# Optimization experiments

Hardware: AMD Instinct MI355X
Metric: run time of the kernel (lower is better)

The kernel has to match this reference:

```python
import math
import jax, jax.numpy as jnp
import numpy as np

S, B, H = 2048, 1, 4096
NH, HD = 32, 128          # heads, head dim
ROT = HD // 2             # rotary dim per 2D-RoPE half = 64


def rotate_half(x):
    x1, x2 = jnp.split(x, 2, axis=-1)
    return jnp.concatenate([-x2, x1], axis=-1)


def rope_tables(seq_len, dim, base=10000.0):
    inv_freq = 1.0 / (base ** (jnp.arange(0, dim, 2, dtype=jnp.float32) / dim))
    freqs = jnp.arange(seq_len, dtype=jnp.float32)[:, None] * inv_freq[None, :]
    emb = jnp.concatenate([freqs, freqs], axis=-1)  # [S, dim]
    return jnp.cos(emb), jnp.sin(emb)


def apply_rope(q, k, cos, sin, pos):
    # q,k: [S,B,NH,ROT]; pos: [S,B] -> gather cos/sin per token
    c = cos[pos][:, :, None, :]  # [S,B,1,ROT]
    s = sin[pos][:, :, None, :]
    return q * c + rotate_half(q) * s, k * c + rotate_half(k) * s


def setup_inputs() -> dict:
    key = jax.random.key(0)
    ks = jax.random.split(key, 5)
    hidden_states = jax.random.normal(ks[0], (S, B, H), dtype=jnp.float32)
    pos = jnp.arange(S, dtype=jnp.int64 if jax.config.jax_enable_x64 else jnp.int32)
    position_ids = jnp.stack([pos, pos])[None]  # [B=1, 2, S]
    attention_mask = jnp.triu(jnp.ones((S, S), dtype=bool), k=1)[None, None]  # True = masked
    scale = 0.02
    wqkv = jax.random.normal(ks[1], (3 * H, H), dtype=jnp.float32) * scale
    bqkv = jax.random.normal(ks[2], (3 * H,), dtype=jnp.float32) * scale
    wdense = jax.random.normal(ks[3], (H, H), dtype=jnp.float32) * scale
    bdense = jax.random.normal(ks[4], (H,), dtype=jnp.float32) * scale
    return {"hidden_states": hidden_states, "position_ids": position_ids,
            "attention_mask": attention_mask, "wqkv": wqkv, "bqkv": bqkv,
            "wdense": wdense, "bdense": bdense, "layer_id": 1}


def reference(hidden_states, position_ids, attention_mask, wqkv, bqkv, wdense, bdense, layer_id):
    s, b, h = hidden_states.shape
    # fused QKV projection: [S,B,NH,3*HD]
    mixed = (jnp.einsum('sbh,oh->sbo', hidden_states, wqkv) + bqkv).reshape(s, b, NH, 3 * HD)
    q, k, v = jnp.split(mixed, 3, axis=-1)  # each [S,B,NH,HD]

    # 2D RoPE: split head dim in half, rotate each half with its own position ids
    q1, q2 = jnp.split(q, 2, axis=-1)
    k1, k2 = jnp.split(k, 2, axis=-1)
    cos, sin = rope_tables(s, ROT)
    pos = position_ids[:, 0, :].T       # [S,B]
    block_pos = position_ids[:, 1, :].T  # [S,B]
    q1, k1 = apply_rope(q1, k1, cos, sin, pos)
    q2, k2 = apply_rope(q2, k2, cos, sin, block_pos)
    q = jnp.concatenate([q1, q2], axis=-1)
    k = jnp.concatenate([k1, k2], axis=-1)

    # layer-scaled attention (ChatGLM style)
    coeff = float(layer_id + 1)
    q = q / (math.sqrt(HD) * coeff)
    scores = jnp.einsum('sbhd,tbhd->bhst', q, k)  # [B,NH,S,S]
    scores = jnp.where(attention_mask, jnp.float32(-10000.0), scores)
    scores = scores.astype(jnp.float32) * coeff
    probs = jax.nn.softmax(scores, axis=-1).astype(q.dtype)
    context = jnp.einsum('bhst,tbhd->sbhd', probs, v).reshape(s, b, h)

    out = jnp.einsum('sbh,oh->sbo', context, wdense) + bdense
    return out
```

## Files before the change

### kernel.cpp

```cpp
#include <hip/hip_runtime.h>

typedef unsigned short u16;
typedef unsigned int u32;
typedef __attribute__((ext_vector_type(4))) float f32x4;
typedef __attribute__((ext_vector_type(8))) short bf16x8;
typedef __attribute__((ext_vector_type(2))) unsigned int u32x2;

#define S_LEN 2048
#define NHEAD 32
#define HDD 128
#define HID 4096
#define N_QKV 12288
#define KDIM 4096
#define RS 12288

__device__ __forceinline__ u16 f2bf(float f) {
  u32 u = __builtin_bit_cast(u32, f);
  u = (u + 0x7FFFu + ((u >> 16) & 1u)) >> 16;
  return (u16)u;
}
__device__ __forceinline__ float bf2f(u16 h) {
  u32 u = ((u32)h) << 16;
  return __builtin_bit_cast(float, u);
}

__device__ __forceinline__ void gl2lds16(const void* g, void* l) {
  __builtin_amdgcn_global_load_lds(
      (const __attribute__((address_space(1))) u32*)g,
      (__attribute__((address_space(3))) u32*)l, 16, 0, 0);
}

#define FULL_BAR()                          \
  {                                         \
    asm volatile("" ::: "memory");          \
    __builtin_amdgcn_s_barrier();           \
    asm volatile("" ::: "memory");          \
  }

__global__ __launch_bounds__(256) void cvt3_kernel(const float* __restrict__ s0, u16* __restrict__ d0, int n0,
                                                   const float* __restrict__ s1, u16* __restrict__ d1, int n1,
                                                   const float* __restrict__ s2, u16* __restrict__ d2, int n2,
                                                   float* __restrict__ cos_t, float* __restrict__ sin_t) {
  int i = blockIdx.x * blockDim.x + threadIdx.x;
  if (i < S_LEN * 32) {
    int s = i >> 5, ii = i & 31;
    float invf = expf(-0.28782313662425572f * (float)ii);
    float a = (float)s * invf;
    cos_t[i] = cosf(a);
    sin_t[i] = sinf(a);
  }
  int st = gridDim.x * blockDim.x;
  int ntot = n0 + n1 + n2;
  for (; i < ntot; i += st) {
    const float* s;
    u16* d;
    int j = i;
    if (j < n0) {
      s = s0; d = d0;
    } else if (j < n0 + n1) {
      j -= n0; s = s1; d = d1;
    } else {
      j -= n0 + n1; s = s2; d = d2;
    }
    float4 v = ((const float4*)s)[j];
    u32x2 o;
    o.x = (u32)f2bf(v.x) | ((u32)f2bf(v.y) << 16);
    o.y = (u32)f2bf(v.z) | ((u32)f2bf(v.w) << 16);
    ((u32x2*)d)[j] = o;
  }
}

__global__ __launch_bounds__(512, 2) void gemmQ(const u16* __restrict__ A,
                                                const u16* __restrict__ B,
                                                const float* __restrict__ bias,
                                                u16* __restrict__ outb) {
  __shared__ __align__(16) char lds[3][40960];

  const int tid = threadIdx.x;
  const int lane = tid & 63, w = tid >> 6;
  const int l15 = lane & 15, g = lane >> 4;
  const int wm = w >> 2, wn = w & 3;

  int x = blockIdx.x & 7, loc = blockIdx.x >> 3;
  int mb = loc & 7, nb = x * 4 + (loc >> 3);
  const int bm = mb * 256, bn = nb * 384;

  f32x4 acc[8][6];
  f32x4 z4 = {0.f, 0.f, 0.f, 0.f};
#pragma unroll
  for (int mi = 0; mi < 8; ++mi)
#pragma unroll
    for (int ni = 0; ni < 6; ++ni) acc[mi][ni] = z4;

  const size_t K2 = (size_t)KDIM * 2;

  const char* gA[2];
#pragma unroll
  for (int j = 0; j < 2; ++j) {
    int slot = j * 512 + tid;
    int line = slot >> 3;
    int sl = (slot & 7) ^ (line & 7);
    int row = 2 * line + (sl >> 2);
    int colb = (sl & 3) * 16;
    gA[j] = (const char*)A + (size_t)(bm + row) * K2 + colb;
  }
  const char* gB[3];
#pragma unroll
  for (int j = 0; j < 3; ++j) {
    int slot = j * 512 + tid;
    int line = slot >> 3;
    int sl = (slot & 7) ^ (line & 7);
    int row = 2 * line + (sl >> 2);
    int colb = (sl & 3) * 16;
    gB[j] = (const char*)B + (size_t)(bn + row) * K2 + colb;
  }
  const int ldst = w * 1024;

#define QIA(t, bi)                                                  \
  {                                                                 \
    char* Lb = lds[bi];                                             \
    gl2lds16(gA[0] + (size_t)(t) * 64, Lb + ldst);                  \
    gl2lds16(gA[1] + (size_t)(t) * 64, Lb + 8192 + ldst);           \
  }
#define QIB(t, bi)                                                  \
  {                                                                 \
    char* Lb = lds[bi] + 16384;                                     \
    _Pragma("unroll")                                               \
    for (int j = 0; j < 3; ++j)                                     \
      gl2lds16(gB[j] + (size_t)(t) * 64, Lb + j * 8192 + ldst);     \
  }

  int offA[8], offB[6];
#pragma unroll
  for (int mi = 0; mi < 8; ++mi) {
    int r = wm * 128 + mi * 16 + l15;
    int line = r >> 1;
    int sl = (((r & 1) << 2) + g) ^ (line & 7);
    offA[mi] = line * 128 + sl * 16;
  }
#pragma unroll
  for (int ni = 0; ni < 6; ++ni) {
    int r = wn * 96 + ni * 16 + l15;
    int line = r >> 1;
    int sl = (((r & 1) << 2) + g) ^ (line & 7);
    offB[ni] = 16384 + line * 128 + sl * 16;
  }

  QIA(0, 0); QIB(0, 0);
  QIA(1, 1); QIB(1, 1);
  asm volatile("s_waitcnt vmcnt(5)" ::: "memory");
  FULL_BAR();

  int cur = 0, nx2 = 2;
  for (int kt = 0; kt < 128; ++kt) {
    const char* buf = lds[cur];
    const bool pf = (kt + 2) < 128;
    bf16x8 a[4], b[6];
#pragma unroll
    for (int mi = 0; mi < 4; ++mi) a[mi] = *(const bf16x8*)(buf + offA[mi]);
#pragma unroll
    for (int ni = 0; ni < 6; ++ni) b[ni] = *(const bf16x8*)(buf + offB[ni]);
    if (pf) QIA(kt + 2, nx2);
    FULL_BAR();
    __builtin_amdgcn_s_setprio(1);
#pragma unroll
    for (int mi = 0; mi < 4; ++mi)
#pragma unroll
      for (int ni = 0; ni < 6; ++ni)
        acc[mi][ni] = __builtin_amdgcn_mfma_f32_16x16x32_bf16(a[mi], b[ni], acc[mi][ni], 0, 0, 0);
    __builtin_amdgcn_s_setprio(0);
#pragma unroll
    for (int mi = 0; mi < 4; ++mi) a[mi] = *(const bf16x8*)(buf + offA[4 + mi]);
    if (pf) {
      QIB(kt + 2, nx2);
      asm volatile("s_waitcnt vmcnt(5)" ::: "memory");
    } else if (kt == 126) {
      asm volatile("s_waitcnt vmcnt(0)" ::: "memory");
    }
    FULL_BAR();
    __builtin_amdgcn_s_setprio(1);
#pragma unroll
    for (int mi = 0; mi < 4; ++mi)
#pragma unroll
      for (int ni = 0; ni < 6; ++ni)
        acc[4 + mi][ni] = __builtin_amdgcn_mfma_f32_16x16x32_bf16(a[mi], b[ni], acc[4 + mi][ni], 0, 0, 0);
    __builtin_amdgcn_s_setprio(0);
    cur = (cur + 1 == 3) ? 0 : cur + 1;
    nx2 = (nx2 + 1 == 3) ? 0 : nx2 + 1;
  }
#undef QIA
#undef QIB

#pragma unroll
  for (int ni = 0; ni < 6; ++ni) {
    int n = bn + wn * 96 + ni * 16 + l15;
    float bv = bias[n];
#pragma unroll
    for (int mi = 0; mi < 8; ++mi) {
      int m0 = bm + wm * 128 + mi * 16 + 4 * g;
#pragma unroll
      for (int rr = 0; rr < 4; ++rr)
        outb[(size_t)(m0 + rr) * N_QKV + n] = f2bf(acc[mi][ni][rr] + bv);
    }
  }
}

template <int NW, int EPI>
__global__ __launch_bounds__(512, 2) void gemmK(const u16* __restrict__ A,
                                                const u16* __restrict__ B,
                                                const float* __restrict__ bias, int N, int NTt,
                                                u16* __restrict__ outb, float* __restrict__ outf) {
  constexpr int BN = 32 * NW;
  constexpr int NLB = NW / 2;
  constexpr int BSUB = BN * 64;
  constexpr int BUFSZ = 32768 + 2 * BSUB;
  __shared__ __align__(16) char lds[2][BUFSZ];

  const int tid = threadIdx.x;
  const int lane = tid & 63, w = tid >> 6;
  const int l15 = lane & 15, g = lane >> 4;
  const int wm = w >> 1, wn = w & 1;

  int perx = gridDim.x >> 3;
  int npx = perx >> 3;
  int x = blockIdx.x & 7, loc = blockIdx.x >> 3;
  int mb = loc & 7, nb = x * npx + (loc >> 3);
  const int bm = mb * 256, bn = nb * BN;

  f32x4 acc[4][NW];
  f32x4 z4 = {0.f, 0.f, 0.f, 0.f};
#pragma unroll
  for (int mi = 0; mi < 4; ++mi)
#pragma unroll
    for (int ni = 0; ni < NW; ++ni) acc[mi][ni] = z4;

  const size_t K2 = (size_t)KDIM * 2;

  const char* gA[2];
#pragma unroll
  for (int j = 0; j < 2; ++j) {
    int slot = j * 512 + tid;
    int line = slot >> 3;
    int sl = (slot & 7) ^ (line & 7);
    int row = 2 * line + (sl >> 2);
    int colb = (sl & 3) * 16;
    gA[j] = (const char*)A + (size_t)(bm + row) * K2 + colb;
  }
  const char* gB[NLB];
#pragma unroll
  for (int j = 0; j < NLB; ++j) {
    int n_ = j * 512 + tid;
    int kkj = (n_ >= 128 * NW) ? 1 : 0;
    int m_ = n_ - kkj * 128 * NW;
    int line = m_ >> 3;
    int sl = (m_ & 7) ^ (line & 7);
    int row = 2 * line + (sl >> 2);
    int colb = (sl & 3) * 16;
    gB[j] = (const char*)B + (size_t)(bn + row) * K2 + kkj * 64 + colb;
  }
  const int ldst = w * 1024;

#define ISSUE_A(t, kk)                                                        \
  {                                                                           \
    char* Lb = lds[(t) & 1] + (kk) * 16384;                                   \
    gl2lds16(gA[0] + (size_t)(t) * 128 + (kk) * 64, Lb + ldst);               \
    gl2lds16(gA[1] + (size_t)(t) * 128 + (kk) * 64, Lb + 8192 + ldst);        \
  }
#define ISSUE_B(t)                                                            \
  {                                                                           \
    char* Lb = lds[(t) & 1] + 32768;                                          \
    _Pragma("unroll")                                                         \
    for (int j = 0; j < NLB; ++j)                                             \
      gl2lds16(gB[j] + (size_t)(t) * 128, Lb + j * 8192 + ldst);              \
  }

  int offA[4], offB[2][NW];
#pragma unroll
  for (int mi = 0; mi < 4; ++mi) {
    int r = wm * 64 + mi * 16 + l15;
    int line = r >> 1;
    int sl = (((r & 1) << 2) + g) ^ (line & 7);
    offA[mi] = line * 128 + sl * 16;
  }
#pragma unroll
  for (int kk = 0; kk < 2; ++kk)
#pragma unroll
    for (int ni = 0; ni < NW; ++ni) {
      int r = wn * (16 * NW) + ni * 16 + l15;
      int line = r >> 1;
      int sl = (((r & 1) << 2) + g) ^ (line & 7);
      offB[kk][ni] = 32768 + kk * BSUB + line * 128 + sl * 16;
    }

  ISSUE_A(0, 0);
  ISSUE_B(0);
  ISSUE_A(0, 1);
  asm volatile("s_waitcnt vmcnt(2)" ::: "memory");
  FULL_BAR();

  for (int kt = 0; kt < NTt; ++kt) {
    const char* buf = lds[kt & 1];
    const bool pf = (kt + 1) < NTt;
    bf16x8 a[4], b[NW];
#pragma unroll
    for (int mi = 0; mi < 4; ++mi) a[mi] = *(const bf16x8*)(buf + offA[mi]);
#pragma unroll
    for (int ni = 0; ni < NW; ++ni) b[ni] = *(const bf16x8*)(buf + offB[0][ni]);
    if (pf) {
      ISSUE_A(kt + 1, 0);
      ISSUE_B(kt + 1);
      asm volatile("s_waitcnt vmcnt(%0)" ::"i"(2 + NLB) : "memory");
    } else {
      asm volatile("s_waitcnt vmcnt(0)" ::: "memory");
    }
    FULL_BAR();
    __builtin_amdgcn_s_setprio(1);
#pragma unroll
    for (int mi = 0; mi < 4; ++mi)
#pragma unroll
      for (int ni = 0; ni < NW; ++ni)
        acc[mi][ni] = __builtin_amdgcn_mfma_f32_16x16x32_bf16(a[mi], b[ni], acc[mi][ni], 0, 0, 0);
    __builtin_amdgcn_s_setprio(0);
#pragma unroll
    for (int mi = 0; mi < 4; ++mi) a[mi] = *(const bf16x8*)(buf + 16384 + offA[mi]);
#pragma unroll
    for (int ni = 0; ni < NW; ++ni) b[ni] = *(const bf16x8*)(buf + offB[1][ni]);
    if (pf) {
      ISSUE_A(kt + 1, 1);
      asm volatile("s_waitcnt vmcnt(2)" ::: "memory");
    }
    FULL_BAR();
    __builtin_amdgcn_s_setprio(1);
#pragma unroll
    for (int mi = 0; mi < 4; ++mi)
#pragma unroll
      for (int ni = 0; ni < NW; ++ni)
        acc[mi][ni] = __builtin_amdgcn_mfma_f32_16x16x32_bf16(a[mi], b[ni], acc[mi][ni], 0, 0, 0);
    __builtin_amdgcn_s_setprio(0);
  }
#undef ISSUE_A
#undef ISSUE_B

#pragma unroll
  for (int ni = 0; ni < NW; ++ni) {
    int n = bn + wn * (16 * NW) + ni * 16 + l15;
    float bv = bias[n];
    if (EPI == 0) {
#pragma unroll
      for (int mi = 0; mi < 4; ++mi) {
        int m0 = bm + wm * 64 + mi * 16 + 4 * g;
#pragma unroll
        for (int rr = 0; rr < 4; ++rr)
          outb[(size_t)(m0 + rr) * N + n] = f2bf(acc[mi][ni][rr] + bv);
      }
    } else {
#pragma unroll
      for (int mi = 0; mi < 4; ++mi) {
        int m0 = bm + wm * 64 + mi * 16 + 4 * g;
#pragma unroll
        for (int rr = 0; rr < 4; ++rr) outf[(size_t)(m0 + rr) * N + n] = acc[mi][ni][rr] + bv;
      }
    }
  }
}

__global__ __launch_bounds__(256) void attn_kernel(const u16* __restrict__ mixed,
                                                   const int* __restrict__ pid,
                                                   const float* __restrict__ cos_t,
                                                   const float* __restrict__ sin_t,
                                                   u16* __restrict__ ctx) {
  __shared__ __align__(16) u16 Ksh[32 * 136];
  __shared__ __align__(16) u16 Vsh[128 * 32];
  __shared__ __align__(16) u16 Pt[4][16 * 40];

  int tid = threadIdx.x;
  int lane = tid & 63, w = tid >> 6;
  int lane15 = lane & 15, g = lane >> 4;

  int bpair = blockIdx.x & 15;
  int h = blockIdx.x >> 4;

  const u16* qp = mixed + (size_t)h * 384;
  const u16* kp = mixed + (size_t)h * 384 + 128;
  const u16* vp = mixed + (size_t)h * 384 + 256;

  int krow = tid >> 3;
  int kc8 = tid & 7;
  int ke0 = (kc8 & 3) * 8 + (kc8 >> 2) * 64;
  int khalf = (kc8 >> 2);
  int ki0 = ke0 & 31;
  int a_ = tid & 15, b_ = tid >> 4;
  f32x4 z4 = {0.f, 0.f, 0.f, 0.f};
  const float QSC = 0.08838834764831845f;

  for (int pass = 0; pass < 2; ++pass) {
    int qi = pass ? (31 - bpair) : bpair;
    int qbase = qi * 64;
    int qrow = qbase + w * 16 + lane15;
    int ntiles = 2 * qi + 2;

    bf16x8 qf[4];
    const u16* qptr = qp + (size_t)qrow * RS + g * 8;
#pragma unroll
    for (int d0 = 0; d0 < 4; ++d0) qf[d0] = *(const bf16x8*)(qptr + d0 * 32);
    {
      int p1 = pid[qrow], p2 = pid[S_LEN + qrow];
      float4 c1a = *(const float4*)(cos_t + p1 * 32 + g * 8);
      float4 c1b = *(const float4*)(cos_t + p1 * 32 + g * 8 + 4);
      float4 s1a = *(const float4*)(sin_t + p1 * 32 + g * 8);
      float4 s1b = *(const float4*)(sin_t + p1 * 32 + g * 8 + 4);
      float4 c2a = *(const float4*)(cos_t + p2 * 32 + g * 8);
      float4 c2b = *(const float4*)(cos_t + p2 * 32 + g * 8 + 4);
      float4 s2a = *(const float4*)(sin_t + p2 * 32 + g * 8);
      float4 s2b = *(const float4*)(sin_t + p2 * 32 + g * 8 + 4);
      float cc[8], ss[8], dd[8], tt[8];
#pragma unroll
      for (int j = 0; j < 4; ++j) {
        cc[j] = ((const float*)&c1a)[j]; cc[4 + j] = ((const float*)&c1b)[j];
        ss[j] = ((const float*)&s1a)[j]; ss[4 + j] = ((const float*)&s1b)[j];
        dd[j] = ((const float*)&c2a)[j]; dd[4 + j] = ((const float*)&c2b)[j];
        tt[j] = ((const float*)&s2a)[j]; tt[4 + j] = ((const float*)&s2b)[j];
      }
#pragma unroll
      for (int j = 0; j < 8; ++j) {
        float x1 = bf2f((u16)qf[0][j]), x2 = bf2f((u16)qf[1][j]);
        qf[0][j] = (short)f2bf((x1 * cc[j] - x2 * ss[j]) * QSC);
        qf[1][j] = (short)f2bf((x2 * cc[j] + x1 * ss[j]) * QSC);
        float y1 = bf2f((u16)qf[2][j]), y2 = bf2f((u16)qf[3][j]);
        qf[2][j] = (short)f2bf((y1 * dd[j] - y2 * tt[j]) * QSC);
        qf[3][j] = (short)f2bf((y2 * dd[j] + y1 * tt[j]) * QSC);
      }
    }

    f32x4 pv[8];
#pragma unroll
    for (int db = 0; db < 8; ++db) pv[db] = z4;
    float m_run = -1e30f, l_run = 0.0f;

    for (int t = 0; t < ntiles; ++t) {
      int kb0 = t * 32;
      __syncthreads();
      {
        int p = pid[khalf * S_LEN + kb0 + krow];
        const u16* rowp = kp + (size_t)(kb0 + krow) * RS;
        bf16x8 x1 = *(const bf16x8*)(rowp + ke0);
        bf16x8 x2 = *(const bf16x8*)(rowp + ke0 + 32);
        float4 ca = *(const float4*)(cos_t + p * 32 + ki0);
        float4 cb = *(const float4*)(cos_t + p * 32 + ki0 + 4);
        float4 sa = *(const float4*)(sin_t + p * 32 + ki0);
        float4 sb = *(const float4*)(sin_t + p * 32 + ki0 + 4);
        bf16x8 o1, o2;
#pragma unroll
        for (int j = 0; j < 8; ++j) {
          float c = (j < 4) ? ((const float*)&ca)[j] : ((const float*)&cb)[j - 4];
          float s = (j < 4) ? ((const float*)&sa)[j] : ((const float*)&sb)[j - 4];
          float v1 = bf2f((u16)x1[j]), v2 = bf2f((u16)x2[j]);
          o1[j] = (short)f2bf(v1 * c - v2 * s);
          o2[j] = (short)f2bf(v2 * c + v1 * s);
        }
        *(bf16x8*)(Ksh + krow * 136 + ke0) = o1;
        *(bf16x8*)(Ksh + krow * 136 + ke0 + 32) = o2;
        int k0 = 2 * a_, d0 = 8 * b_;
        bf16x8 r0 = *(const bf16x8*)(vp + (size_t)(kb0 + k0) * RS + d0);
        bf16x8 r1 = *(const bf16x8*)(vp + (size_t)(kb0 + k0 + 1) * RS + d0);
#pragma unroll
        for (int jj = 0; jj < 8; ++jj) {
          int d = d0 + jj;
          u32 val = (u32)(u16)r0[jj] | ((u32)(u16)r1[jj] << 16);
          *(u32*)(Vsh + d * 32 + (((k0 >> 3) ^ (d & 3)) << 3) + (k0 & 7)) = val;
        }
      }
      __syncthreads();

      f32x4 sa0 = z4, sa1 = z4;
#pragma unroll
      for (int d0 = 0; d0 < 4; ++d0) {
        bf16x8 k0f = *(const bf16x8*)(Ksh + lane15 * 136 + d0 * 32 + g * 8);
        bf16x8 k1f = *(const bf16x8*)(Ksh + (16 + lane15) * 136 + d0 * 32 + g * 8);
        sa0 = __builtin_amdgcn_mfma_f32_16x16x32_bf16(k0f, qf[d0], sa0, 0, 0, 0);
        sa1 = __builtin_amdgcn_mfma_f32_16x16x32_bf16(k1f, qf[d0], sa1, 0, 0, 0);
      }
      float s[8];
#pragma unroll
      for (int rr = 0; rr < 4; ++rr) {
        int kg0 = kb0 + 4 * g + rr;
        int kg1 = kb0 + 16 + 4 * g + rr;
        s[rr] = (kg0 > qrow) ? -1e30f : sa0[rr];
        s[4 + rr] = (kg1 > qrow) ? -1e30f : sa1[rr];
      }
      float mx = s[0];
#pragma unroll
      for (int i2 = 1; i2 < 8; ++i2) mx = fmaxf(mx, s[i2]);
      mx = fmaxf(mx, __shfl_xor(mx, 16));
      mx = fmaxf(mx, __shfl_xor(mx, 32));
      float mnew = fmaxf(m_run, mx);
      float fac = exp2f((m_run - mnew) * 1.4426950408889634f);
      float p[8], psum = 0.f;
#pragma unroll
      for (int i2 = 0; i2 < 8; ++i2) {
        p[i2] = exp2f((s[i2] - mnew) * 1.4426950408889634f);
        psum += p[i2];
      }
      psum += __shfl_xor(psum, 16);
      psum += __shfl_xor(psum, 32);
      l_run = l_run * fac + psum;
      m_run = mnew;
#pragma unroll
      for (int db = 0; db < 8; ++db) pv[db] *= fac;

      u32 w0 = (u32)f2bf(p[0]) | ((u32)f2bf(p[1]) << 16);
      u32 w1 = (u32)f2bf(p[2]) | ((u32)f2bf(p[3]) << 16);
      u32 w2 = (u32)f2bf(p[4]) | ((u32)f2bf(p[5]) << 16);
      u32 w3 = (u32)f2bf(p[6]) | ((u32)f2bf(p[7]) << 16);
      u32x2 pa, pb;
      pa.x = w0; pa.y = w1; pb.x = w2; pb.y = w3;
      *(u32x2*)(&Pt[w][lane15 * 40 + 4 * g]) = pa;
      *(u32x2*)(&Pt[w][lane15 * 40 + 16 + 4 * g]) = pb;
      asm volatile("s_waitcnt lgkmcnt(0)" ::: "memory");
      bf16x8 pfrag = *(const bf16x8*)(&Pt[w][lane15 * 40 + 8 * g]);

#pragma unroll
      for (int db = 0; db < 8; ++db) {
        int d = db * 16 + lane15;
        bf16x8 vf = *(const bf16x8*)(Vsh + d * 32 + ((g ^ (d & 3)) << 3));
        pv[db] = __builtin_amdgcn_mfma_f32_16x16x32_bf16(vf, pfrag, pv[db], 0, 0, 0);
      }
    }

    float inv = 1.0f / l_run;
#pragma unroll
    for (int db = 0; db < 8; ++db) {
      ushort4 o;
      o.x = f2bf(pv[db][0] * inv);
      o.y = f2bf(pv[db][1] * inv);
      o.z = f2bf(pv[db][2] * inv);
      o.w = f2bf(pv[db][3] * inv);
      *(ushort4*)(ctx + (size_t)qrow * HID + h * HDD + db * 16 + 4 * g) = o;
    }
    __syncthreads();
  }
}

extern "C" void kernel_launch(void* const* d_in, const int* in_sizes, int n_in,
                              void* d_out, int out_size, void* d_ws, size_t ws_size,
                              hipStream_t stream) {
  const float* hidden = (const float*)d_in[0];
  const int* pid = (const int*)d_in[1];
  const float* wqkv = (const float*)d_in[3];
  const float* bqkv = (const float*)d_in[4];
  const float* wdense = (const float*)d_in[5];
  const float* bdense = (const float*)d_in[6];
  float* out = (float*)d_out;

  char* ws = (char*)d_ws;
  u16* W1 = (u16*)ws;
  u16* W2 = (u16*)(ws + 100663296);
  u16* X = (u16*)(ws + 134217728);
  u16* mixed = (u16*)(ws + 150994944);
  u16* ctx = (u16*)(ws + 201326592);
  float* cos_t = (float*)(ws + 218103808);
  float* sin_t = (float*)(ws + 218365952);

  cvt3_kernel<<<dim3(2048), dim3(256), 0, stream>>>(
      wqkv, W1, N_QKV * KDIM / 4, wdense, W2, HID * KDIM / 4, hidden, X, S_LEN * HID / 4,
      cos_t, sin_t);

  gemmQ<<<dim3(256), dim3(512), 0, stream>>>(X, W1, bqkv, mixed);

  attn_kernel<<<dim3(512), dim3(256), 0, stream>>>(mixed, pid, cos_t, sin_t, ctx);

  gemmK<4, 1><<<dim3(256), dim3(512), 0, stream>>>(
      ctx, W2, bdense, HID, 64, nullptr, out);
}
```

Measured before the change: 497.3 us.

## Fuse dense weight conversion into output GEMM, precompute K RoPE, widen attention tiles

Drops the separate fp32-to-bf16 conversion of the dense weight and has the output GEMM load fp32 B tiles, round them to bf16 in registers and write them to LDS itself. Moves RoPE for K out of the attention kernel into a dedicated in-place pass over the QKV buffer. Attention now processes 64-key tiles instead of 32, which halves the number of tile iterations and barriers. The aim is to remove the weight-conversion round trip and the repeated per-tile K rotation, at the cost of an extra kernel launch, more fp32 traffic and conversion ALU inside the GEMM main loop, and larger LDS use in attention.

```diff
diff --git a/kernel.cpp b/kernel.cpp
--- a/kernel.cpp
+++ b/kernel.cpp
@@ -38,7 +38,6 @@
   }
 
 __global__ __launch_bounds__(256) void cvt3_kernel(const float* __restrict__ s0, u16* __restrict__ d0, int n0,
-                                                   const float* __restrict__ s1, u16* __restrict__ d1, int n1,
                                                    const float* __restrict__ s2, u16* __restrict__ d2, int n2,
                                                    float* __restrict__ cos_t, float* __restrict__ sin_t) {
   int i = blockIdx.x * blockDim.x + threadIdx.x;
@@ -50,17 +49,15 @@
     sin_t[i] = sinf(a);
   }
   int st = gridDim.x * blockDim.x;
-  int ntot = n0 + n1 + n2;
+  int ntot = n0 + n2;
   for (; i < ntot; i += st) {
     const float* s;
     u16* d;
     int j = i;
     if (j < n0) {
       s = s0; d = d0;
-    } else if (j < n0 + n1) {
-      j -= n0; s = s1; d = d1;
     } else {
-      j -= n0 + n1; s = s2; d = d2;
+      j -= n0; s = s2; d = d2;
     }
     float4 v = ((const float4*)s)[j];
     u32x2 o;
@@ -68,6 +65,49 @@
     o.y = (u32)f2bf(v.z) | ((u32)f2bf(v.w) << 16);
     ((u32x2*)d)[j] = o;
   }
+}
+
+__global__ __launch_bounds__(256) void ropek_kernel(u16* __restrict__ mixed,
+                                                    const int* __restrict__ pid,
+                                                    const float* __restrict__ cos_t,
+                                                    const float* __restrict__ sin_t) {
+  int idx = blockIdx.x * blockDim.x + threadIdx.x;
+  const int total = NHEAD * S_LEN * 2 * 8;
+  if (idx >= total) return;
+  int j = idx & 7;
+  int half = (idx >> 3) & 1;
+  int s = (idx >> 4) & (S_LEN - 1);
+  int h = idx >> 15;
+  int i0 = j * 4;
+  int p = pid[half * S_LEN + s];
+  float4 c4 = *(const float4*)(cos_t + p * 32 + i0);
+  float4 s4 = *(const float4*)(sin_t + p * 32 + i0);
+  u16* base = mixed + (size_t)s * RS + h * 384 + 128 + half * 64 + i0;
+  ushort4 x1v = *(const ushort4*)(base);
+  ushort4 x2v = *(const ushort4*)(base + 32);
+  ushort4 o1, o2;
+  {
+    float x1 = bf2f(x1v.x), x2 = bf2f(x2v.x);
+    o1.x = f2bf(x1 * c4.x - x2 * s4.x);
+    o2.x = f2bf(x2 * c4.x + x1 * s4.x);
+  }
+  {
+    float x1 = bf2f(x1v.y), x2 = bf2f(x2v.y);
+    o1.y = f2bf(x1 * c4.y - x2 * s4.y);
+    o2.y = f2bf(x2 * c4.y + x1 * s4.y);
+  }
+  {
+    float x1 = bf2f(x1v.z), x2 = bf2f(x2v.z);
+    o1.z = f2bf(x1 * c4.z - x2 * s4.z);
+    o2.z = f2bf(x2 * c4.z + x1 * s4.z);
+  }
+  {
+    float x1 = bf2f(x1v.w), x2 = bf2f(x2v.w);
+    o1.w = f2bf(x1 * c4.w - x2 * s4.w);
+    o2.w = f2bf(x2 * c4.w + x1 * s4.w);
+  }
+  *(ushort4*)(base) = o1;
+  *(ushort4*)(base + 32) = o2;
 }
 
 __global__ __launch_bounds__(512, 2) void gemmQ(const u16* __restrict__ A,
@@ -205,34 +245,27 @@
   }
 }
 
-template <int NW, int EPI>
-__global__ __launch_bounds__(512, 2) void gemmK(const u16* __restrict__ A,
-                                                const u16* __restrict__ B,
-                                                const float* __restrict__ bias, int N, int NTt,
-                                                u16* __restrict__ outb, float* __restrict__ outf) {
-  constexpr int BN = 32 * NW;
-  constexpr int NLB = NW / 2;
-  constexpr int BSUB = BN * 64;
-  constexpr int BUFSZ = 32768 + 2 * BSUB;
-  __shared__ __align__(16) char lds[2][BUFSZ];
+__global__ __launch_bounds__(512, 2) void gemmD(const u16* __restrict__ A,
+                                                const float* __restrict__ Bf,
+                                                const float* __restrict__ bias,
+                                                float* __restrict__ outf) {
+  __shared__ __align__(16) char lds[2][49152];
 
   const int tid = threadIdx.x;
   const int lane = tid & 63, w = tid >> 6;
   const int l15 = lane & 15, g = lane >> 4;
   const int wm = w >> 1, wn = w & 1;
 
-  int perx = gridDim.x >> 3;
-  int npx = perx >> 3;
   int x = blockIdx.x & 7, loc = blockIdx.x >> 3;
-  int mb = loc & 7, nb = x * npx + (loc >> 3);
-  const int bm = mb * 256, bn = nb * BN;
-
-  f32x4 acc[4][NW];
+  int mb = loc & 7, nb = x * 4 + (loc >> 3);
+  const int bm = mb * 256, bn = nb * 128;
+
+  f32x4 acc[4][4];
   f32x4 z4 = {0.f, 0.f, 0.f, 0.f};
 #pragma unroll
   for (int mi = 0; mi < 4; ++mi)
 #pragma unroll
-    for (int ni = 0; ni < NW; ++ni) acc[mi][ni] = z4;
+    for (int ni = 0; ni < 4; ++ni) acc[mi][ni] = z4;
 
   const size_t K2 = (size_t)KDIM * 2;
 
@@ -246,35 +279,46 @@
     int colb = (sl & 3) * 16;
     gA[j] = (const char*)A + (size_t)(bm + row) * K2 + colb;
   }
-  const char* gB[NLB];
-#pragma unroll
-  for (int j = 0; j < NLB; ++j) {
-    int n_ = j * 512 + tid;
-    int kkj = (n_ >= 128 * NW) ? 1 : 0;
-    int m_ = n_ - kkj * 128 * NW;
-    int line = m_ >> 3;
-    int sl = (m_ & 7) ^ (line & 7);
-    int row = 2 * line + (sl >> 2);
-    int colb = (sl & 3) * 16;
-    gB[j] = (const char*)B + (size_t)(bn + row) * K2 + kkj * 64 + colb;
-  }
+  int bline = tid >> 3;
+  int bsl = tid & 7;
+  int brow = 2 * bline + (bsl >> 2);
+  int bcole = (bsl & 3) * 8;
+  const float* gBs = Bf + (size_t)(bn + brow) * KDIM + bcole;
+  int bphys = bsl ^ (bline & 7);
+  const int bwr = 32768 + bline * 128 + bphys * 16;
   const int ldst = w * 1024;
 
-#define ISSUE_A(t, kk)                                                        \
+#define DIA(t, kk)                                                            \
   {                                                                           \
     char* Lb = lds[(t) & 1] + (kk) * 16384;                                   \
     gl2lds16(gA[0] + (size_t)(t) * 128 + (kk) * 64, Lb + ldst);               \
     gl2lds16(gA[1] + (size_t)(t) * 128 + (kk) * 64, Lb + 8192 + ldst);        \
   }
-#define ISSUE_B(t)                                                            \
+#define DGB(t)                                                                \
   {                                                                           \
-    char* Lb = lds[(t) & 1] + 32768;                                          \
-    _Pragma("unroll")                                                         \
-    for (int j = 0; j < NLB; ++j)                                             \
-      gl2lds16(gB[j] + (size_t)(t) * 128, Lb + j * 8192 + ldst);              \
-  }
-
-  int offA[4], offB[2][NW];
+    const float* p0 = gBs + (size_t)(t) * 64;                                 \
+    b0a = *(const float4*)(p0);                                               \
+    b0b = *(const float4*)(p0 + 4);                                           \
+    b1a = *(const float4*)(p0 + 32);                                          \
+    b1b = *(const float4*)(p0 + 36);                                          \
+  }
+#define DWB(t)                                                                \
+  {                                                                           \
+    bf16x8 o0, o1;                                                            \
+    o0[0] = (short)f2bf(b0a.x); o0[1] = (short)f2bf(b0a.y);                   \
+    o0[2] = (short)f2bf(b0a.z); o0[3] = (short)f2bf(b0a.w);                   \
+    o0[4] = (short)f2bf(b0b.x); o0[5] = (short)f2bf(b0b.y);                   \
+    o0[6] = (short)f2bf(b0b.z); o0[7] = (short)f2bf(b0b.w);                   \
+    o1[0] = (short)f2bf(b1a.x); o1[1] = (short)f2bf(b1a.y);                   \
+    o1[2] = (short)f2bf(b1a.z); o1[3] = (short)f2bf(b1a.w);                   \
+    o1[4] = (short)f2bf(b1b.x); o1[5] = (short)f2bf(b1b.y);                   \
+    o1[6] = (short)f2bf(b1b.z); o1[7] = (short)f2bf(b1b.w);                   \
+    char* Lb = lds[(t) & 1];                                                  \
+    *(bf16x8*)(Lb + bwr) = o0;                                                \
+    *(bf16x8*)(Lb + 8192 + bwr) = o1;                                         \
+  }
+
+  int offA[4], offB[2][4];
 #pragma unroll
   for (int mi = 0; mi < 4; ++mi) {
     int r = wm * 64 + mi * 16 + l15;
@@ -285,31 +329,34 @@
 #pragma unroll
   for (int kk = 0; kk < 2; ++kk)
 #pragma unroll
-    for (int ni = 0; ni < NW; ++ni) {
-      int r = wn * (16 * NW) + ni * 16 + l15;
+    for (int ni = 0; ni < 4; ++ni) {
+      int r = wn * 64 + ni * 16 + l15;
       int line = r >> 1;
       int sl = (((r & 1) << 2) + g) ^ (line & 7);
-      offB[kk][ni] = 32768 + kk * BSUB + line * 128 + sl * 16;
-    }
-
-  ISSUE_A(0, 0);
-  ISSUE_B(0);
-  ISSUE_A(0, 1);
-  asm volatile("s_waitcnt vmcnt(2)" ::: "memory");
+      offB[kk][ni] = 32768 + kk * 8192 + line * 128 + sl * 16;
+    }
+
+  float4 b0a, b0b, b1a, b1b;
+  DGB(0);
+  DIA(0, 0);
+  DIA(0, 1);
+  asm volatile("s_waitcnt vmcnt(4)" ::: "memory");
+  DWB(0);
+  asm volatile("s_waitcnt vmcnt(0) lgkmcnt(0)" ::: "memory");
   FULL_BAR();
 
-  for (int kt = 0; kt < NTt; ++kt) {
+  for (int kt = 0; kt < 64; ++kt) {
     const char* buf = lds[kt & 1];
-    const bool pf = (kt + 1) < NTt;
-    bf16x8 a[4], b[NW];
+    const bool pf = (kt + 1) < 64;
+    bf16x8 a[4], b[4];
 #pragma unroll
     for (int mi = 0; mi < 4; ++mi) a[mi] = *(const bf16x8*)(buf + offA[mi]);
 #pragma unroll
-    for (int ni = 0; ni < NW; ++ni) b[ni] = *(const bf16x8*)(buf + offB[0][ni]);
+    for (int ni = 0; ni < 4; ++ni) b[ni] = *(const bf16x8*)(buf + offB[0][ni]);
     if (pf) {
-      ISSUE_A(kt + 1, 0);
-      ISSUE_B(kt + 1);
-      asm volatile("s_waitcnt vmcnt(%0)" ::"i"(2 + NLB) : "memory");
+      DIA(kt + 1, 0);
+      DGB(kt + 1);
+      asm volatile("s_waitcnt vmcnt(6)" ::: "memory");
     } else {
       asm volatile("s_waitcnt vmcnt(0)" ::: "memory");
     }
@@ -318,48 +365,41 @@
 #pragma unroll
     for (int mi = 0; mi < 4; ++mi)
 #pragma unroll
-      for (int ni = 0; ni < NW; ++ni)
+      for (int ni = 0; ni < 4; ++ni)
         acc[mi][ni] = __builtin_amdgcn_mfma_f32_16x16x32_bf16(a[mi], b[ni], acc[mi][ni], 0, 0, 0);
     __builtin_amdgcn_s_setprio(0);
 #pragma unroll
     for (int mi = 0; mi < 4; ++mi) a[mi] = *(const bf16x8*)(buf + 16384 + offA[mi]);
 #pragma unroll
-    for (int ni = 0; ni < NW; ++ni) b[ni] = *(const bf16x8*)(buf + offB[1][ni]);
+    for (int ni = 0; ni < 4; ++ni) b[ni] = *(const bf16x8*)(buf + offB[1][ni]);
     if (pf) {
-      ISSUE_A(kt + 1, 1);
+      DIA(kt + 1, 1);
       asm volatile("s_waitcnt vmcnt(2)" ::: "memory");
+      DWB(kt + 1);
+      asm volatile("s_waitcnt lgkmcnt(0)" ::: "memory");
     }
     FULL_BAR();
     __builtin_amdgcn_s_setprio(1);
 #pragma unroll
     for (int mi = 0; mi < 4; ++mi)
 #pragma unroll
-      for (int ni = 0; ni < NW; ++ni)
+      for (int ni = 0; ni < 4; ++ni)
         acc[mi][ni] = __builtin_amdgcn_mfma_f32_16x16x32_bf16(a[mi], b[ni], acc[mi][ni], 0, 0, 0);
     __builtin_amdgcn_s_setprio(0);
   }
-#undef ISSUE_A
-#undef ISSUE_B
-
-#pragma unroll
-  for (int ni = 0; ni < NW; ++ni) {
-    int n = bn + wn * (16 * NW) + ni * 16 + l15;
+#undef DIA
+#undef DGB
+#undef DWB
+
+#pragma unroll
+  for (int ni = 0; ni < 4; ++ni) {
+    int n = bn + wn * 64 + ni * 16 + l15;
     float bv = bias[n];
-    if (EPI == 0) {
-#pragma unroll
-      for (int mi = 0; mi < 4; ++mi) {
-        int m0 = bm + wm * 64 + mi * 16 + 4 * g;
-#pragma unroll
-        for (int rr = 0; rr < 4; ++rr)
-          outb[(size_t)(m0 + rr) * N + n] = f2bf(acc[mi][ni][rr] + bv);
-      }
-    } else {
-#pragma unroll
-      for (int mi = 0; mi < 4; ++mi) {
-        int m0 = bm + wm * 64 + mi * 16 + 4 * g;
-#pragma unroll
-        for (int rr = 0; rr < 4; ++rr) outf[(size_t)(m0 + rr) * N + n] = acc[mi][ni][rr] + bv;
-      }
+#pragma unroll
+    for (int mi = 0; mi < 4; ++mi) {
+      int m0 = bm + wm * 64 + mi * 16 + 4 * g;
+#pragma unroll
+      for (int rr = 0; rr < 4; ++rr) outf[(size_t)(m0 + rr) * HID + n] = acc[mi][ni][rr] + bv;
     }
   }
 }
@@ -369,9 +409,9 @@
                                                    const float* __restrict__ cos_t,
                                                    const float* __restrict__ sin_t,
                                                    u16* __restrict__ ctx) {
-  __shared__ __align__(16) u16 Ksh[32 * 136];
-  __shared__ __align__(16) u16 Vsh[128 * 32];
-  __shared__ __align__(16) u16 Pt[4][16 * 40];
+  __shared__ __align__(16) u16 Ksh[64 * 136];
+  __shared__ __align__(16) u16 Vsh[128 * 64];
+  __shared__ __align__(16) u16 Pt[4][16 * 72];
 
   int tid = threadIdx.x;
   int lane = tid & 63, w = tid >> 6;
@@ -384,20 +424,17 @@
   const u16* kp = mixed + (size_t)h * 384 + 128;
   const u16* vp = mixed + (size_t)h * 384 + 256;
 
-  int krow = tid >> 3;
-  int kc8 = tid & 7;
-  int ke0 = (kc8 & 3) * 8 + (kc8 >> 2) * 64;
-  int khalf = (kc8 >> 2);
-  int ki0 = ke0 & 31;
-  int a_ = tid & 15, b_ = tid >> 4;
+  int krow = tid >> 2, kc = (tid & 3) * 32;
+  int vk0 = 2 * (tid & 31), vd0 = (tid >> 5) * 16;
   f32x4 z4 = {0.f, 0.f, 0.f, 0.f};
   const float QSC = 0.08838834764831845f;
+  const float L2E = 1.4426950408889634f;
 
   for (int pass = 0; pass < 2; ++pass) {
     int qi = pass ? (31 - bpair) : bpair;
     int qbase = qi * 64;
     int qrow = qbase + w * 16 + lane15;
-    int ntiles = 2 * qi + 2;
+    int ntiles = qi + 1;
 
     bf16x8 qf[4];
     const u16* qptr = qp + (size_t)qrow * RS + g * 8;
@@ -405,21 +442,13 @@
     for (int d0 = 0; d0 < 4; ++d0) qf[d0] = *(const bf16x8*)(qptr + d0 * 32);
     {
       int p1 = pid[qrow], p2 = pid[S_LEN + qrow];
-      float4 c1a = *(const float4*)(cos_t + p1 * 32 + g * 8);
-      float4 c1b = *(const float4*)(cos_t + p1 * 32 + g * 8 + 4);
-      float4 s1a = *(const float4*)(sin_t + p1 * 32 + g * 8);
-      float4 s1b = *(const float4*)(sin_t + p1 * 32 + g * 8 + 4);
-      float4 c2a = *(const float4*)(cos_t + p2 * 32 + g * 8);
-      float4 c2b = *(const float4*)(cos_t + p2 * 32 + g * 8 + 4);
-      float4 s2a = *(const float4*)(sin_t + p2 * 32 + g * 8);
-      float4 s2b = *(const float4*)(sin_t + p2 * 32 + g * 8 + 4);
       float cc[8], ss[8], dd[8], tt[8];
 #pragma unroll
-      for (int j = 0; j < 4; ++j) {
-        cc[j] = ((const float*)&c1a)[j]; cc[4 + j] = ((const float*)&c1b)[j];
-        ss[j] = ((const float*)&s1a)[j]; ss[4 + j] = ((const float*)&s1b)[j];
-        dd[j] = ((const float*)&c2a)[j]; dd[4 + j] = ((const float*)&c2b)[j];
-        tt[j] = ((const float*)&s2a)[j]; tt[4 + j] = ((const float*)&s2b)[j];
+      for (int j = 0; j < 8; ++j) {
+        cc[j] = cos_t[p1 * 32 + g * 8 + j];
+        ss[j] = sin_t[p1 * 32 + g * 8 + j];
+        dd[j] = cos_t[p2 * 32 + g * 8 + j];
+        tt[j] = sin_t[p2 * 32 + g * 8 + j];
       }
 #pragma unroll
       for (int j = 0; j < 8; ++j) {
@@ -438,67 +467,58 @@
     float m_run = -1e30f, l_run = 0.0f;
 
     for (int t = 0; t < ntiles; ++t) {
-      int kb0 = t * 32;
+      int kb0 = t * 64;
       __syncthreads();
       {
-        int p = pid[khalf * S_LEN + kb0 + krow];
-        const u16* rowp = kp + (size_t)(kb0 + krow) * RS;
-        bf16x8 x1 = *(const bf16x8*)(rowp + ke0);
-        bf16x8 x2 = *(const bf16x8*)(rowp + ke0 + 32);
-        float4 ca = *(const float4*)(cos_t + p * 32 + ki0);
-        float4 cb = *(const float4*)(cos_t + p * 32 + ki0 + 4);
-        float4 sa = *(const float4*)(sin_t + p * 32 + ki0);
-        float4 sb = *(const float4*)(sin_t + p * 32 + ki0 + 4);
-        bf16x8 o1, o2;
-#pragma unroll
-        for (int j = 0; j < 8; ++j) {
-          float c = (j < 4) ? ((const float*)&ca)[j] : ((const float*)&cb)[j - 4];
-          float s = (j < 4) ? ((const float*)&sa)[j] : ((const float*)&sb)[j - 4];
-          float v1 = bf2f((u16)x1[j]), v2 = bf2f((u16)x2[j]);
-          o1[j] = (short)f2bf(v1 * c - v2 * s);
-          o2[j] = (short)f2bf(v2 * c + v1 * s);
-        }
-        *(bf16x8*)(Ksh + krow * 136 + ke0) = o1;
-        *(bf16x8*)(Ksh + krow * 136 + ke0 + 32) = o2;
-        int k0 = 2 * a_, d0 = 8 * b_;
-        bf16x8 r0 = *(const bf16x8*)(vp + (size_t)(kb0 + k0) * RS + d0);
-        bf16x8 r1 = *(const bf16x8*)(vp + (size_t)(kb0 + k0 + 1) * RS + d0);
+        const bf16x8* src = (const bf16x8*)(kp + (size_t)(kb0 + krow) * RS + kc);
+#pragma unroll
+        for (int c = 0; c < 4; ++c)
+          *(bf16x8*)(Ksh + krow * 136 + kc + c * 8) = src[c];
+        const bf16x8* r0p = (const bf16x8*)(vp + (size_t)(kb0 + vk0) * RS + vd0);
+        const bf16x8* r1p = (const bf16x8*)(vp + (size_t)(kb0 + vk0 + 1) * RS + vd0);
+        bf16x8 r00 = r0p[0], r01 = r0p[1];
+        bf16x8 r10 = r1p[0], r11 = r1p[1];
 #pragma unroll
         for (int jj = 0; jj < 8; ++jj) {
-          int d = d0 + jj;
-          u32 val = (u32)(u16)r0[jj] | ((u32)(u16)r1[jj] << 16);
-          *(u32*)(Vsh + d * 32 + (((k0 >> 3) ^ (d & 3)) << 3) + (k0 & 7)) = val;
+          int d = vd0 + jj;
+          u32 v0 = (u32)(u16)r00[jj] | ((u32)(u16)r10[jj] << 16);
+          *(u32*)((char*)Vsh + d * 128 + (((vk0 >> 3) ^ (d & 7)) << 4) + (vk0 & 7) * 2) = v0;
+          int d2 = vd0 + 8 + jj;
+          u32 v1 = (u32)(u16)r01[jj] | ((u32)(u16)r11[jj] << 16);
+          *(u32*)((char*)Vsh + d2 * 128 + (((vk0 >> 3) ^ (d2 & 7)) << 4) + (vk0 & 7) * 2) = v1;
         }
       }
       __syncthreads();
 
-      f32x4 sa0 = z4, sa1 = z4;
-#pragma unroll
-      for (int d0 = 0; d0 < 4; ++d0) {
-        bf16x8 k0f = *(const bf16x8*)(Ksh + lane15 * 136 + d0 * 32 + g * 8);
-        bf16x8 k1f = *(const bf16x8*)(Ksh + (16 + lane15) * 136 + d0 * 32 + g * 8);
-        sa0 = __builtin_amdgcn_mfma_f32_16x16x32_bf16(k0f, qf[d0], sa0, 0, 0, 0);
-        sa1 = __builtin_amdgcn_mfma_f32_16x16x32_bf16(k1f, qf[d0], sa1, 0, 0, 0);
-      }
-      float s[8];
-#pragma unroll
-      for (int rr = 0; rr < 4; ++rr) {
-        int kg0 = kb0 + 4 * g + rr;
-        int kg1 = kb0 + 16 + 4 * g + rr;
-        s[rr] = (kg0 > qrow) ? -1e30f : sa0[rr];
-        s[4 + rr] = (kg1 > qrow) ? -1e30f : sa1[rr];
-      }
+      f32x4 sa[4];
+#pragma unroll
+      for (int kt16 = 0; kt16 < 4; ++kt16) sa[kt16] = z4;
+#pragma unroll
+      for (int kt16 = 0; kt16 < 4; ++kt16)
+#pragma unroll
+        for (int d0 = 0; d0 < 4; ++d0) {
+          bf16x8 kf = *(const bf16x8*)(Ksh + (kt16 * 16 + lane15) * 136 + d0 * 32 + g * 8);
+          sa[kt16] = __builtin_amdgcn_mfma_f32_16x16x32_bf16(kf, qf[d0], sa[kt16], 0, 0, 0);
+        }
+      float s[16];
+#pragma unroll
+      for (int kt16 = 0; kt16 < 4; ++kt16)
+#pragma unroll
+        for (int rr = 0; rr < 4; ++rr) {
+          int kg = kb0 + kt16 * 16 + 4 * g + rr;
+          s[kt16 * 4 + rr] = (kg > qrow) ? -1e30f : sa[kt16][rr];
+        }
       float mx = s[0];
 #pragma unroll
-      for (int i2 = 1; i2 < 8; ++i2) mx = fmaxf(mx, s[i2]);
+      for (int i2 = 1; i2 < 16; ++i2) mx = fmaxf(mx, s[i2]);
       mx = fmaxf(mx, __shfl_xor(mx, 16));
       mx = fmaxf(mx, __shfl_xor(mx, 32));
       float mnew = fmaxf(m_run, mx);
-      float fac = exp2f((m_run - mnew) * 1.4426950408889634f);
-      float p[8], psum = 0.f;
-#pragma unroll
-      for (int i2 = 0; i2 < 8; ++i2) {
-        p[i2] = exp2f((s[i2] - mnew) * 1.4426950408889634f);
+      float fac = exp2f((m_run - mnew) * L2E);
+      float p[16], psum = 0.f;
+#pragma unroll
+      for (int i2 = 0; i2 < 16; ++i2) {
+        p[i2] = exp2f((s[i2] - mnew) * L2E);
         psum += p[i2];
       }
       psum += __shfl_xor(psum, 16);
@@ -508,22 +528,24 @@
 #pragma unroll
       for (int db = 0; db < 8; ++db) pv[db] *= fac;
 
-      u32 w0 = (u32)f2bf(p[0]) | ((u32)f2bf(p[1]) << 16);
-      u32 w1 = (u32)f2bf(p[2]) | ((u32)f2bf(p[3]) << 16);
-      u32 w2 = (u32)f2bf(p[4]) | ((u32)f2bf(p[5]) << 16);
-      u32 w3 = (u32)f2bf(p[6]) | ((u32)f2bf(p[7]) << 16);
-      u32x2 pa, pb;
-      pa.x = w0; pa.y = w1; pb.x = w2; pb.y = w3;
-      *(u32x2*)(&Pt[w][lane15 * 40 + 4 * g]) = pa;
-      *(u32x2*)(&Pt[w][lane15 * 40 + 16 + 4 * g]) = pb;
+#pragma unroll
+      for (int kt16 = 0; kt16 < 4; ++kt16) {
+        u32x2 pw;
+        pw.x = (u32)f2bf(p[kt16 * 4 + 0]) | ((u32)f2bf(p[kt16 * 4 + 1]) << 16);
+        pw.y = (u32)f2bf(p[kt16 * 4 + 2]) | ((u32)f2bf(p[kt16 * 4 + 3]) << 16);
+        *(u32x2*)(&Pt[w][lane15 * 72 + kt16 * 16 + 4 * g]) = pw;
+      }
       asm volatile("s_waitcnt lgkmcnt(0)" ::: "memory");
-      bf16x8 pfrag = *(const bf16x8*)(&Pt[w][lane15 * 40 + 8 * g]);
+      bf16x8 pf0 = *(const bf16x8*)(&Pt[w][lane15 * 72 + 8 * g]);
+      bf16x8 pf1 = *(const bf16x8*)(&Pt[w][lane15 * 72 + 32 + 8 * g]);
 
 #pragma unroll
       for (int db = 0; db < 8; ++db) {
         int d = db * 16 + lane15;
-        bf16x8 vf = *(const bf16x8*)(Vsh + d * 32 + ((g ^ (d & 3)) << 3));
-        pv[db] = __builtin_amdgcn_mfma_f32_16x16x32_bf16(vf, pfrag, pv[db], 0, 0, 0);
+        bf16x8 vf0 = *(const bf16x8*)((const char*)Vsh + d * 128 + ((g ^ (d & 7)) << 4));
+        bf16x8 vf1 = *(const bf16x8*)((const char*)Vsh + d * 128 + (((4 + g) ^ (d & 7)) << 4));
+        pv[db] = __builtin_amdgcn_mfma_f32_16x16x32_bf16(vf0, pf0, pv[db], 0, 0, 0);
+        pv[db] = __builtin_amdgcn_mfma_f32_16x16x32_bf16(vf1, pf1, pv[db], 0, 0, 0);
       }
     }
 
@@ -554,7 +576,6 @@
 
   char* ws = (char*)d_ws;
   u16* W1 = (u16*)ws;
-  u16* W2 = (u16*)(ws + 100663296);
   u16* X = (u16*)(ws + 134217728);
   u16* mixed = (u16*)(ws + 150994944);
   u16* ctx = (u16*)(ws + 201326592);
@@ -562,13 +583,13 @@
   float* sin_t = (float*)(ws + 218365952);
 
   cvt3_kernel<<<dim3(2048), dim3(256), 0, stream>>>(
-      wqkv, W1, N_QKV * KDIM / 4, wdense, W2, HID * KDIM / 4, hidden, X, S_LEN * HID / 4,
-      cos_t, sin_t);
+      wqkv, W1, N_QKV * KDIM / 4, hidden, X, S_LEN * HID / 4, cos_t, sin_t);
 
   gemmQ<<<dim3(256), dim3(512), 0, stream>>>(X, W1, bqkv, mixed);
 
+  ropek_kernel<<<dim3(4096), dim3(256), 0, stream>>>(mixed, pid, cos_t, sin_t);
+
   attn_kernel<<<dim3(512), dim3(256), 0, stream>>>(mixed, pid, cos_t, sin_t, ctx);
 
-  gemmK<4, 1><<<dim3(256), dim3(512), 0, stream>>>(
-      ctx, W2, bdense, HID, 64, nullptr, out);
-}
+  gemmD<<<dim3(256), dim3(512), 0, stream>>>(ctx, wdense, bdense, out);
+}
```

New measurement: 492.9 us. Within noise of the previous version (-0.9%).
